# Kernel optimization log

Hardware: AMD Instinct MI355X
Metric: run time of the kernel (lower is better)

Reference implementation:

```python
import jax, jax.numpy as jnp
import numpy as np

EMBED_DIM = 1024
NUM_HEADS = 16
HEAD_DIM = EMBED_DIM // NUM_HEADS
BATCH = 2
SEQ = 2048


def setup_inputs() -> dict:
    key = jax.random.key(0)
    ks = jax.random.split(key, 9)
    s = 1.0 / np.sqrt(EMBED_DIM)
    return {
        "x": jax.random.normal(ks[0], (BATCH, SEQ, EMBED_DIM), jnp.float32),
        "mask": jnp.ones((BATCH, SEQ), jnp.int32),
        "Wq": jax.random.normal(ks[1], (EMBED_DIM, EMBED_DIM), jnp.float32) * s,
        "bq": jax.random.normal(ks[2], (EMBED_DIM,), jnp.float32) * s,
        "Wk": jax.random.normal(ks[3], (EMBED_DIM, EMBED_DIM), jnp.float32) * s,
        "bk": jax.random.normal(ks[4], (EMBED_DIM,), jnp.float32) * s,
        "Wv": jax.random.normal(ks[5], (EMBED_DIM, EMBED_DIM), jnp.float32) * s,
        "bv": jax.random.normal(ks[6], (EMBED_DIM,), jnp.float32) * s,
        "Wo": jax.random.normal(ks[7], (EMBED_DIM, EMBED_DIM), jnp.float32) * s,
        "bo": jax.random.normal(ks[8], (EMBED_DIM,), jnp.float32) * s,
    }


def reference(x, mask, Wq, bq, Wk, bk, Wv, bv, Wo, bo):
    B, S, E = x.shape
    H, D = NUM_HEADS, HEAD_DIM
    # torch Linear: y = x @ W.T + b
    q = (x @ Wq.T + bq).reshape(B, S, H, D).transpose(0, 2, 1, 3)  # [B,H,S,D]
    k = (x @ Wk.T + bk).reshape(B, S, H, D).transpose(0, 2, 1, 3)
    v = (x @ Wv.T + bv).reshape(B, S, H, D).transpose(0, 2, 1, 3)
    scores = jnp.einsum("bhqd,bhkd->bhqk", q, k) / jnp.sqrt(jnp.float32(D))
    # mask: [B,S] -> [B,1,1,S]; fill masked positions with -1e9
    scores = jnp.where(mask[:, None, None, :] == 0, jnp.float32(-1e9), scores)
    probs = jax.nn.softmax(scores, axis=-1)
    # dropout omitted: original stores a float and would crash; eval semantics = identity
    attn = jnp.einsum("bhqk,bhkd->bhqd", probs, v)  # [B,H,S,D]
    attn = attn.transpose(0, 2, 1, 3).reshape(B, S, E)
    return attn @ Wo.T + bo
```

## Files before the change

kernel.cpp:

```cpp
#include <hip/hip_runtime.h>
#include <stdint.h>

#define S_LEN 2048
#define EMB   1024
#define NH    16
#define HD    64
#define BK 64

typedef __bf16 bf16x8 __attribute__((ext_vector_type(8)));
typedef short  short4v __attribute__((ext_vector_type(4)));
typedef unsigned int uint2v __attribute__((ext_vector_type(2)));
typedef float  floatx4 __attribute__((ext_vector_type(4)));

#if defined(__has_builtin)
#if __has_builtin(__builtin_amdgcn_mfma_f32_16x16x16bf16_1k)
#define HAVE_MFMA16 1
#endif
#if __has_builtin(__builtin_amdgcn_exp2f)
#define EXP2F __builtin_amdgcn_exp2f
#endif
#endif
#ifndef EXP2F
#define EXP2F exp2f
#endif

#define QSCALE 0.1803368801111204f

__device__ __forceinline__ unsigned short f2bf(float f) {
  unsigned u = __builtin_bit_cast(unsigned, f);
  u += 0x7fffu + ((u >> 16) & 1u);
  return (unsigned short)(u >> 16);
}
__device__ __forceinline__ unsigned short f2bf_hu(float f) {
  return (unsigned short)((__builtin_bit_cast(unsigned, f) + 0x8000u) >> 16);
}
__device__ __forceinline__ unsigned packbf2(float a, float b) {
  unsigned ua = __builtin_bit_cast(unsigned, a) + 0x8000u;
  unsigned ub = __builtin_bit_cast(unsigned, b) + 0x8000u;
  return __builtin_amdgcn_perm(ub, ua, 0x07060302);
}

__global__ __launch_bounds__(256) void cvt_all(const float* __restrict__ x,
                                               const float* __restrict__ Wq,
                                               const float* __restrict__ Wk,
                                               const float* __restrict__ Wv,
                                               const float* __restrict__ Wo,
                                               unsigned short* __restrict__ xb,
                                               unsigned short* __restrict__ Wqb,
                                               unsigned short* __restrict__ Wkb,
                                               unsigned short* __restrict__ Wvb,
                                               unsigned short* __restrict__ Wob) {
  int blk = blockIdx.x;
  const float* s; unsigned short* d; int off;
  if (blk < 4096)      { s = x;  d = xb;  off = blk; }
  else if (blk < 5120) { s = Wq; d = Wqb; off = blk - 4096; }
  else if (blk < 6144) { s = Wk; d = Wkb; off = blk - 5120; }
  else if (blk < 7168) { s = Wv; d = Wvb; off = blk - 6144; }
  else                 { s = Wo; d = Wob; off = blk - 7168; }
  int i = (off * 256 + threadIdx.x) * 4;
  float4 v = *(const float4*)(s + i);
  ushort4 o;
  o.x = f2bf(v.x); o.y = f2bf(v.y); o.z = f2bf(v.z); o.w = f2bf(v.w);
  *(ushort4*)(d + i) = o;
}

__device__ __forceinline__ void stage16(const void* g, void* l) {
  __builtin_amdgcn_global_load_lds(
      (const __attribute__((address_space(1))) void*)g,
      (__attribute__((address_space(3))) void*)l, 16, 0, 0);
}

__global__ __launch_bounds__(256, 3) void qkv_gemm(const unsigned short* __restrict__ xb,
                                                   const unsigned short* __restrict__ Wqb,
                                                   const unsigned short* __restrict__ Wkb,
                                                   const unsigned short* __restrict__ Wvb,
                                                   const float* __restrict__ bq,
                                                   const float* __restrict__ bk,
                                                   const float* __restrict__ bv,
                                                   unsigned short* __restrict__ Qb,
                                                   unsigned short* __restrict__ Kb,
                                                   unsigned short* __restrict__ Vtb) {
  __shared__ unsigned short As[128 * BK];
  __shared__ unsigned short Bs[128 * BK];
  const int z = blockIdx.z;
  const unsigned short* Bm = (z == 0) ? Wqb : (z == 1) ? Wkb : Wvb;
  const float* bias        = (z == 0) ? bq  : (z == 1) ? bk  : bv;
  unsigned short* outp     = (z == 0) ? Qb  : (z == 1) ? Kb  : Vtb;
  const float scale = (z == 0) ? QSCALE : 1.0f;
  const int mode = (z == 2) ? 2 : 1;

  const int tid  = threadIdx.x;
  const int lane = tid & 63;
  const int wave = tid >> 6;
  const int m16  = lane & 15;
  const int quad = lane >> 4;
  const int m0 = blockIdx.x * 128;
  const int n0 = blockIdx.y * 128;
  const int wrow = (wave >> 1) * 64;
  const int wcol = (wave & 1) * 64;
  const int K = 1024;

  floatx4 acc[4][4];
  for (int i = 0; i < 4; ++i)
    for (int j = 0; j < 4; ++j) acc[i][j] = floatx4{0.f, 0.f, 0.f, 0.f};

  for (int k0 = 0; k0 < K; k0 += BK) {
    __syncthreads();
    for (int i = 0; i < 4; ++i) {
      int c = i * 256 + tid;
      int row = c >> 3, col = (c & 7) << 3;
      stage16(xb + (size_t)(m0 + row) * K + k0 + col,
              (char*)As + (size_t)(i * 256 + wave * 64) * 16);
      stage16(Bm + (size_t)(n0 + row) * K + k0 + col,
              (char*)Bs + (size_t)(i * 256 + wave * 64) * 16);
    }
    __syncthreads();
    for (int kk = 0; kk < 2; ++kk) {
      bf16x8 af[4], bfr[4];
      for (int ti = 0; ti < 4; ++ti)
        af[ti] = *(const bf16x8*)(As + (wrow + ti * 16 + m16) * BK + kk * 32 + quad * 8);
      for (int tj = 0; tj < 4; ++tj)
        bfr[tj] = *(const bf16x8*)(Bs + (wcol + tj * 16 + m16) * BK + kk * 32 + quad * 8);
      for (int ti = 0; ti < 4; ++ti)
        for (int tj = 0; tj < 4; ++tj)
          acc[ti][tj] = __builtin_amdgcn_mfma_f32_16x16x32_bf16(bfr[tj], af[ti], acc[ti][tj], 0, 0, 0);
    }
  }

  if (mode == 1) {
    for (int ti = 0; ti < 4; ++ti) {
      int m = m0 + wrow + ti * 16 + m16;
      int b = m >> 11, ss = m & 2047;
      for (int tj = 0; tj < 4; ++tj) {
        int n = n0 + wcol + tj * 16 + quad * 4;
        int hh = n >> 6, d = n & 63;
        float4 b4 = *(const float4*)(bias + n);
        float v0 = (acc[ti][tj][0] + b4.x) * scale;
        float v1 = (acc[ti][tj][1] + b4.y) * scale;
        float v2 = (acc[ti][tj][2] + b4.z) * scale;
        float v3 = (acc[ti][tj][3] + b4.w) * scale;
        uint2v pk{packbf2(v0, v1), packbf2(v2, v3)};
        *(uint2v*)((unsigned short*)outp +
                   ((size_t)(b * NH + hh) * S_LEN + ss) * HD + d) = pk;
      }
    }
  } else {
    for (int tj = 0; tj < 4; ++tj)
      for (int reg = 0; reg < 4; ++reg) {
        int n = n0 + wcol + tj * 16 + quad * 4 + reg;
        int hh = n >> 6, d = n & 63;
        float bv = bias[n];
        for (int ti = 0; ti < 4; ++ti) {
          int m = m0 + wrow + ti * 16 + m16;
          int b = m >> 11, ss = m & 2047;
          ((unsigned short*)outp)[((size_t)(b * NH + hh) * HD + d) * S_LEN + ss] =
              f2bf_hu(acc[ti][tj][reg] + bv);
        }
      }
  }
}

__global__ __launch_bounds__(256, 4) void out_gemm(const unsigned short* __restrict__ Ab,
                                                   const unsigned short* __restrict__ Wob,
                                                   const float* __restrict__ bo,
                                                   float* __restrict__ out) {
  __shared__ unsigned short As[128 * BK];
  __shared__ unsigned short Bs[64 * BK];
  const int tid  = threadIdx.x;
  const int lane = tid & 63;
  const int wave = tid >> 6;
  const int m16  = lane & 15;
  const int quad = lane >> 4;
  const int m0 = blockIdx.x * 128;
  const int n0 = blockIdx.y * 64;
  const int wrow = (wave >> 1) * 64;
  const int wcol = (wave & 1) * 32;
  const int K = 1024, N = 1024;

  floatx4 acc[4][2];
  for (int i = 0; i < 4; ++i)
    for (int j = 0; j < 2; ++j) acc[i][j] = floatx4{0.f, 0.f, 0.f, 0.f};

  for (int k0 = 0; k0 < K; k0 += BK) {
    __syncthreads();
    for (int i = 0; i < 4; ++i) {
      int c = i * 256 + tid;
      int row = c >> 3, col = (c & 7) << 3;
      stage16(Ab + (size_t)(m0 + row) * K + k0 + col,
              (char*)As + (size_t)(i * 256 + wave * 64) * 16);
    }
    for (int i = 0; i < 2; ++i) {
      int c = i * 256 + tid;
      int row = c >> 3, col = (c & 7) << 3;
      stage16(Wob + (size_t)(n0 + row) * K + k0 + col,
              (char*)Bs + (size_t)(i * 256 + wave * 64) * 16);
    }
    __syncthreads();
    for (int kk = 0; kk < 2; ++kk) {
      bf16x8 af[4], bfr[2];
      for (int ti = 0; ti < 4; ++ti)
        af[ti] = *(const bf16x8*)(As + (wrow + ti * 16 + m16) * BK + kk * 32 + quad * 8);
      for (int tj = 0; tj < 2; ++tj)
        bfr[tj] = *(const bf16x8*)(Bs + (wcol + tj * 16 + m16) * BK + kk * 32 + quad * 8);
      for (int ti = 0; ti < 4; ++ti)
        for (int tj = 0; tj < 2; ++tj)
          acc[ti][tj] = __builtin_amdgcn_mfma_f32_16x16x32_bf16(af[ti], bfr[tj], acc[ti][tj], 0, 0, 0);
    }
  }

  for (int tj = 0; tj < 2; ++tj) {
    int n = n0 + wcol + tj * 16 + m16;
    float bv = bo[n];
    for (int ti = 0; ti < 4; ++ti)
      for (int reg = 0; reg < 4; ++reg) {
        int m = m0 + wrow + ti * 16 + quad * 4 + reg;
        out[(size_t)m * N + n] = acc[ti][tj][reg] + bv;
      }
  }
}

__global__ __launch_bounds__(256, 2) void attn_kernel(const unsigned short* __restrict__ Qb,
                                                      const unsigned short* __restrict__ Kb,
                                                      const unsigned short* __restrict__ Vtb,
                                                      const int* __restrict__ mask,
                                                      unsigned short* __restrict__ attnb) {
  __shared__ unsigned short Ks[2 * 128 * 64];
  __shared__ unsigned short Vts[2 * 64 * 128];
  __shared__ int zw[4];
#ifndef HAVE_MFMA16
  __shared__ unsigned short Pq[4 * 16 * 72];
#endif

  const int tid  = threadIdx.x;
  const int lane = tid & 63;
  const int wave = tid >> 6;
  const int m16  = lane & 15;
  const int quad = lane >> 4;
  const int bh = blockIdx.x;
  const int qt = blockIdx.y;
  const int b  = bh >> 4;
  const int h  = bh & 15;
  const int q0 = qt * 128;
  const size_t head = (size_t)bh * S_LEN * HD;

  bf16x8 qf[2][2];
  for (int qs = 0; qs < 2; ++qs) {
    const unsigned short* qrow = Qb + head + (size_t)(q0 + wave * 32 + qs * 16 + m16) * HD;
    qf[qs][0] = *(const bf16x8*)(qrow + quad * 8);
    qf[qs][1] = *(const bf16x8*)(qrow + 32 + quad * 8);
  }

  const int kr = lane >> 3, kc = lane & 7;
  const unsigned short* kg0 = Kb + head + (size_t)(wave * 32 + kr) * HD + ((kc ^ (kr & 7)) << 3);
  const int vd = lane >> 4;
  const int vce = (lane & 8) | ((lane & 7) ^ vd);
  const unsigned short* vg0 = Vtb + head + (size_t)(wave * 16 + vd) * S_LEN + (vce << 3);
  const unsigned short* vg1 = Vtb + head + (size_t)(wave * 16 + 4 + vd) * S_LEN + ((vce ^ 4) << 3);
  const int* mrow = mask + b * S_LEN;

#define STAGE_KV(pp, kb_)                                                      \
  {                                                                            \
    const unsigned short* ksrc = kg0 + (size_t)(kb_) * 128 * HD;               \
    char* kdst = (char*)Ks + (pp) * 16384 + wave * 4096;                       \
    stage16(ksrc,        kdst);                                                \
    stage16(ksrc + 512,  kdst + 1024);                                         \
    stage16(ksrc + 1024, kdst + 2048);                                         \
    stage16(ksrc + 1536, kdst + 3072);                                         \
    const unsigned short* ve = vg0 + (kb_) * 128;                              \
    const unsigned short* vo = vg1 + (kb_) * 128;                              \
    char* vdst = (char*)Vts + (pp) * 16384 + wave * 4096;                      \
    stage16(ve,             vdst);                                             \
    stage16(vo,             vdst + 1024);                                      \
    stage16(ve + 8 * S_LEN, vdst + 2048);                                      \
    stage16(vo + 8 * S_LEN, vdst + 3072);                                      \
  }

  float l_run[2] = {0.f, 0.f};
  floatx4 acc_o[2][4];
  for (int qs = 0; qs < 2; ++qs)
    for (int ti = 0; ti < 4; ++ti) acc_o[qs][ti] = floatx4{0.f, 0.f, 0.f, 0.f};

  {
    const int4* mp = (const int4*)(mrow + tid * 8);
    int4 a = mp[0], c4 = mp[1];
    bool z = (a.x & a.y & a.z & a.w & c4.x & c4.y & c4.z & c4.w) == 0;
    unsigned long long bal = __ballot(z);
    if (lane == 0) zw[wave] = (bal != 0ull) ? 1 : 0;
  }

  STAGE_KV(0, 0);
  __syncthreads();
  const bool anymask = (zw[0] | zw[1] | zw[2] | zw[3]) != 0;

  const int xs = m16 & 7;
  const floatx4 fz = floatx4{0.f, 0.f, 0.f, 0.f};

  for (int kb = 0; kb < 16; ++kb) {
    const int p = kb & 1;
    const unsigned short* Kp = Ks + p * (128 * 64);
    const unsigned short* Vp = Vts + p * (64 * 128);
    if (kb < 15) STAGE_KV(p ^ 1, kb + 1);

    for (int hf = 0; hf < 2; ++hf) {
      floatx4 acc_s[2][4];
      {
        bf16x8 kf[4];
        for (int tj = 0; tj < 4; ++tj)
          kf[tj] = *(const bf16x8*)&Kp[(hf * 64 + tj * 16 + m16) * 64 + ((quad ^ xs) << 3)];
        for (int tj = 0; tj < 4; ++tj) {
          acc_s[0][tj] = __builtin_amdgcn_mfma_f32_16x16x32_bf16(kf[tj], qf[0][0], fz, 0, 0, 0);
          acc_s[1][tj] = __builtin_amdgcn_mfma_f32_16x16x32_bf16(kf[tj], qf[1][0], fz, 0, 0, 0);
        }
        for (int tj = 0; tj < 4; ++tj)
          kf[tj] = *(const bf16x8*)&Kp[(hf * 64 + tj * 16 + m16) * 64 + (((4 + quad) ^ xs) << 3)];
        for (int tj = 0; tj < 4; ++tj) {
          acc_s[0][tj] = __builtin_amdgcn_mfma_f32_16x16x32_bf16(kf[tj], qf[0][1], acc_s[0][tj], 0, 0, 0);
          acc_s[1][tj] = __builtin_amdgcn_mfma_f32_16x16x32_bf16(kf[tj], qf[1][1], acc_s[1][tj], 0, 0, 0);
        }
      }

      unsigned up[2][8];
      for (int qs = 0; qs < 2; ++qs) {
        float sv[16];
        for (int t = 0; t < 4; ++t)
          for (int r = 0; r < 4; ++r) sv[t * 4 + r] = acc_s[qs][t][r];
        if (anymask) {
          for (int t = 0; t < 4; ++t)
            for (int r = 0; r < 4; ++r) {
              int idx = kb * 128 + hf * 64 + t * 16 + quad * 4 + r;
              sv[t * 4 + r] += (mrow[idx] == 0) ? -1e9f : 0.f;
            }
        }
        float sl = 0.f;
        for (int i = 0; i < 8; ++i) {
          float p0 = EXP2F(sv[2 * i]);
          float p1 = EXP2F(sv[2 * i + 1]);
          sl += p0 + p1;
          up[qs][i] = packbf2(p0, p1);
        }
        sl += __shfl_xor(sl, 16);
        sl += __shfl_xor(sl, 32);
        l_run[qs] += sl;
      }

#ifdef HAVE_MFMA16
      for (int ti = 0; ti < 4; ++ti)
        for (int c = 0; c < 4; ++c) {
          short4v vf = *(const short4v*)&Vp[(ti * 16 + m16) * 128 +
                                            (((hf * 8 + 2 * c + (quad >> 1)) ^ xs) << 3) +
                                            ((quad & 1) << 2)];
          short4v Pb0 = __builtin_bit_cast(short4v, uint2v{up[0][2 * c], up[0][2 * c + 1]});
          short4v Pb1 = __builtin_bit_cast(short4v, uint2v{up[1][2 * c], up[1][2 * c + 1]});
          acc_o[0][ti] = __builtin_amdgcn_mfma_f32_16x16x16bf16_1k(vf, Pb0, acc_o[0][ti], 0, 0, 0);
          acc_o[1][ti] = __builtin_amdgcn_mfma_f32_16x16x16bf16_1k(vf, Pb1, acc_o[1][ti], 0, 0, 0);
        }
#else
      {
        unsigned short* Pw = Pq + wave * 16 * 72;
        for (int qs = 0; qs < 2; ++qs) {
          for (int t = 0; t < 4; ++t) {
            *(unsigned*)&Pw[m16 * 72 + t * 16 + quad * 4]     = up[qs][2 * t];
            *(unsigned*)&Pw[m16 * 72 + t * 16 + quad * 4 + 2] = up[qs][2 * t + 1];
          }
          for (int kk = 0; kk < 2; ++kk) {
            bf16x8 pf = *(const bf16x8*)&Pw[m16 * 72 + kk * 32 + quad * 8];
            for (int ti = 0; ti < 4; ++ti) {
              bf16x8 vfb = *(const bf16x8*)&Vp[(ti * 16 + m16) * 128 +
                                               (((hf * 8 + kk * 4 + quad) ^ xs) << 3)];
              acc_o[qs][ti] = __builtin_amdgcn_mfma_f32_16x16x32_bf16(vfb, pf, acc_o[qs][ti], 0, 0, 0);
            }
          }
        }
      }
#endif
    }

    __syncthreads();
  }

  for (int qs = 0; qs < 2; ++qs) {
    float rl = 1.f / l_run[qs];
    int orow = q0 + wave * 32 + qs * 16 + m16;
    for (int ti = 0; ti < 4; ++ti) {
      ushort4 o;
      o.x = f2bf_hu(acc_o[qs][ti][0] * rl);
      o.y = f2bf_hu(acc_o[qs][ti][1] * rl);
      o.z = f2bf_hu(acc_o[qs][ti][2] * rl);
      o.w = f2bf_hu(acc_o[qs][ti][3] * rl);
      int e = h * HD + ti * 16 + quad * 4;
      *(ushort4*)&attnb[((size_t)(b * S_LEN + orow)) * EMB + e] = o;
    }
  }
#undef STAGE_KV
}

extern "C" void kernel_launch(void* const* d_in, const int* in_sizes, int n_in,
                              void* d_out, int out_size, void* d_ws, size_t ws_size,
                              hipStream_t stream) {
  const float* x  = (const float*)d_in[0];
  const int* mask = (const int*)d_in[1];
  const float* Wq = (const float*)d_in[2];
  const float* bq = (const float*)d_in[3];
  const float* Wk = (const float*)d_in[4];
  const float* bk = (const float*)d_in[5];
  const float* Wv = (const float*)d_in[6];
  const float* bv = (const float*)d_in[7];
  const float* Wo = (const float*)d_in[8];
  const float* bo = (const float*)d_in[9];
  float* out = (float*)d_out;

  char* ws = (char*)d_ws;
  unsigned short* xb  = (unsigned short*)(ws);
  unsigned short* Wqb = (unsigned short*)(ws + 8388608);
  unsigned short* Wkb = (unsigned short*)(ws + 10485760);
  unsigned short* Wvb = (unsigned short*)(ws + 12582912);
  unsigned short* Wob = (unsigned short*)(ws + 14680064);
  unsigned short* Qb  = (unsigned short*)(ws + 16777216);
  unsigned short* Kbb = (unsigned short*)(ws + 25165824);
  unsigned short* Vtb = (unsigned short*)(ws + 33554432);
  unsigned short* Ab  = (unsigned short*)(ws + 41943040);

  cvt_all<<<dim3(8192), dim3(256), 0, stream>>>(x, Wq, Wk, Wv, Wo, xb, Wqb, Wkb, Wvb, Wob);
  qkv_gemm<<<dim3(32, 8, 3), dim3(256), 0, stream>>>(xb, Wqb, Wkb, Wvb, bq, bk, bv, Qb, Kbb, Vtb);
  attn_kernel<<<dim3(32, 16), dim3(256), 0, stream>>>(Qb, Kbb, Vtb, mask, Ab);
  out_gemm<<<dim3(32, 16), dim3(256), 0, stream>>>(Ab, Wob, bo, out);
}
```

Measured before the change: 197.2 us.

## Shrink attention KV tile to 64 keys to raise occupancy to four blocks per CU

The attention kernel now stages 64-key K/V tiles instead of 128, which halves its shared memory, and its launch bounds ask for 4 blocks per CU instead of 2. The inner half-tile loop is removed, the swizzled staging addresses are simplified, and the per-tile row-sum shuffles are moved so the row sum is reduced once at the end. The aim is more waves in flight to hide latency and fewer cross-lane reductions. In exchange there are twice as many __syncthreads barriers, and the tighter register budget may cause spills.

```diff
diff --git a/kernel.cpp b/kernel.cpp
--- a/kernel.cpp
+++ b/kernel.cpp
@@ -219,13 +219,13 @@
   }
 }
 
-__global__ __launch_bounds__(256, 2) void attn_kernel(const unsigned short* __restrict__ Qb,
+__global__ __launch_bounds__(256, 4) void attn_kernel(const unsigned short* __restrict__ Qb,
                                                       const unsigned short* __restrict__ Kb,
                                                       const unsigned short* __restrict__ Vtb,
                                                       const int* __restrict__ mask,
                                                       unsigned short* __restrict__ attnb) {
-  __shared__ unsigned short Ks[2 * 128 * 64];
-  __shared__ unsigned short Vts[2 * 64 * 128];
+  __shared__ unsigned short Ks[2 * 64 * 64];
+  __shared__ unsigned short Vts[2 * 64 * 64];
   __shared__ int zw[4];
 #ifndef HAVE_MFMA16
   __shared__ unsigned short Pq[4 * 16 * 72];
@@ -251,28 +251,20 @@
   }
 
   const int kr = lane >> 3, kc = lane & 7;
-  const unsigned short* kg0 = Kb + head + (size_t)(wave * 32 + kr) * HD + ((kc ^ (kr & 7)) << 3);
-  const int vd = lane >> 4;
-  const int vce = (lane & 8) | ((lane & 7) ^ vd);
-  const unsigned short* vg0 = Vtb + head + (size_t)(wave * 16 + vd) * S_LEN + (vce << 3);
-  const unsigned short* vg1 = Vtb + head + (size_t)(wave * 16 + 4 + vd) * S_LEN + ((vce ^ 4) << 3);
+  const unsigned short* kg0 = Kb + head + (size_t)(wave * 16 + kr) * HD + ((kc ^ kr) << 3);
+  const unsigned short* vg0 = Vtb + head + (size_t)(wave * 16 + kr) * S_LEN + ((kc ^ kr) << 3);
   const int* mrow = mask + b * S_LEN;
 
 #define STAGE_KV(pp, kb_)                                                      \
   {                                                                            \
-    const unsigned short* ksrc = kg0 + (size_t)(kb_) * 128 * HD;               \
-    char* kdst = (char*)Ks + (pp) * 16384 + wave * 4096;                       \
-    stage16(ksrc,        kdst);                                                \
-    stage16(ksrc + 512,  kdst + 1024);                                         \
-    stage16(ksrc + 1024, kdst + 2048);                                         \
-    stage16(ksrc + 1536, kdst + 3072);                                         \
-    const unsigned short* ve = vg0 + (kb_) * 128;                              \
-    const unsigned short* vo = vg1 + (kb_) * 128;                              \
-    char* vdst = (char*)Vts + (pp) * 16384 + wave * 4096;                      \
-    stage16(ve,             vdst);                                             \
-    stage16(vo,             vdst + 1024);                                      \
-    stage16(ve + 8 * S_LEN, vdst + 2048);                                      \
-    stage16(vo + 8 * S_LEN, vdst + 3072);                                      \
+    const unsigned short* ksrc = kg0 + (size_t)(kb_) * 64 * HD;                \
+    char* kdst = (char*)Ks + (pp) * 8192 + wave * 2048;                        \
+    stage16(ksrc,           kdst);                                             \
+    stage16(ksrc + 8 * HD,  kdst + 1024);                                      \
+    const unsigned short* vsrc = vg0 + (kb_) * 64;                             \
+    char* vdst = (char*)Vts + (pp) * 8192 + wave * 2048;                       \
+    stage16(vsrc,              vdst);                                          \
+    stage16(vsrc + 8 * S_LEN,  vdst + 1024);                                   \
   }
 
   float l_run[2] = {0.f, 0.f};
@@ -295,90 +287,85 @@
   const int xs = m16 & 7;
   const floatx4 fz = floatx4{0.f, 0.f, 0.f, 0.f};
 
-  for (int kb = 0; kb < 16; ++kb) {
+  for (int kb = 0; kb < 32; ++kb) {
     const int p = kb & 1;
-    const unsigned short* Kp = Ks + p * (128 * 64);
-    const unsigned short* Vp = Vts + p * (64 * 128);
-    if (kb < 15) STAGE_KV(p ^ 1, kb + 1);
-
-    for (int hf = 0; hf < 2; ++hf) {
-      floatx4 acc_s[2][4];
-      {
-        bf16x8 kf[4];
-        for (int tj = 0; tj < 4; ++tj)
-          kf[tj] = *(const bf16x8*)&Kp[(hf * 64 + tj * 16 + m16) * 64 + ((quad ^ xs) << 3)];
-        for (int tj = 0; tj < 4; ++tj) {
-          acc_s[0][tj] = __builtin_amdgcn_mfma_f32_16x16x32_bf16(kf[tj], qf[0][0], fz, 0, 0, 0);
-          acc_s[1][tj] = __builtin_amdgcn_mfma_f32_16x16x32_bf16(kf[tj], qf[1][0], fz, 0, 0, 0);
+    const unsigned short* Kp = Ks + p * 4096;
+    const unsigned short* Vp = Vts + p * 4096;
+    if (kb < 31) STAGE_KV(p ^ 1, kb + 1);
+
+    floatx4 acc_s[2][4];
+    {
+      bf16x8 kf[4];
+      for (int tj = 0; tj < 4; ++tj)
+        kf[tj] = *(const bf16x8*)&Kp[(tj * 16 + m16) * 64 + ((quad ^ xs) << 3)];
+      for (int tj = 0; tj < 4; ++tj) {
+        acc_s[0][tj] = __builtin_amdgcn_mfma_f32_16x16x32_bf16(kf[tj], qf[0][0], fz, 0, 0, 0);
+        acc_s[1][tj] = __builtin_amdgcn_mfma_f32_16x16x32_bf16(kf[tj], qf[1][0], fz, 0, 0, 0);
+      }
+      for (int tj = 0; tj < 4; ++tj)
+        kf[tj] = *(const bf16x8*)&Kp[(tj * 16 + m16) * 64 + (((4 + quad) ^ xs) << 3)];
+      for (int tj = 0; tj < 4; ++tj) {
+        acc_s[0][tj] = __builtin_amdgcn_mfma_f32_16x16x32_bf16(kf[tj], qf[0][1], acc_s[0][tj], 0, 0, 0);
+        acc_s[1][tj] = __builtin_amdgcn_mfma_f32_16x16x32_bf16(kf[tj], qf[1][1], acc_s[1][tj], 0, 0, 0);
+      }
+    }
+
+    unsigned up[2][8];
+    for (int qs = 0; qs < 2; ++qs) {
+      if (anymask) {
+        for (int t = 0; t < 4; ++t)
+          for (int r = 0; r < 4; ++r) {
+            int idx = kb * 64 + t * 16 + quad * 4 + r;
+            acc_s[qs][t][r] += (mrow[idx] == 0) ? -1e9f : 0.f;
+          }
+      }
+      float sl = 0.f;
+      for (int i = 0; i < 8; ++i) {
+        float p0 = EXP2F(acc_s[qs][i >> 1][(i & 1) * 2]);
+        float p1 = EXP2F(acc_s[qs][i >> 1][(i & 1) * 2 + 1]);
+        sl += p0 + p1;
+        up[qs][i] = packbf2(p0, p1);
+      }
+      l_run[qs] += sl;
+    }
+
+#ifdef HAVE_MFMA16
+    for (int ti = 0; ti < 4; ++ti)
+      for (int c = 0; c < 4; ++c) {
+        short4v vf = *(const short4v*)&Vp[(ti * 16 + m16) * 64 +
+                                          (((2 * c + (quad >> 1)) ^ xs) << 3) +
+                                          ((quad & 1) << 2)];
+        short4v Pb0 = __builtin_bit_cast(short4v, uint2v{up[0][2 * c], up[0][2 * c + 1]});
+        short4v Pb1 = __builtin_bit_cast(short4v, uint2v{up[1][2 * c], up[1][2 * c + 1]});
+        acc_o[0][ti] = __builtin_amdgcn_mfma_f32_16x16x16bf16_1k(vf, Pb0, acc_o[0][ti], 0, 0, 0);
+        acc_o[1][ti] = __builtin_amdgcn_mfma_f32_16x16x16bf16_1k(vf, Pb1, acc_o[1][ti], 0, 0, 0);
+      }
+#else
+    {
+      unsigned short* Pw = Pq + wave * 16 * 72;
+      for (int qs = 0; qs < 2; ++qs) {
+        for (int t = 0; t < 4; ++t) {
+          *(unsigned*)&Pw[m16 * 72 + t * 16 + quad * 4]     = up[qs][2 * t];
+          *(unsigned*)&Pw[m16 * 72 + t * 16 + quad * 4 + 2] = up[qs][2 * t + 1];
         }
-        for (int tj = 0; tj < 4; ++tj)
-          kf[tj] = *(const bf16x8*)&Kp[(hf * 64 + tj * 16 + m16) * 64 + (((4 + quad) ^ xs) << 3)];
-        for (int tj = 0; tj < 4; ++tj) {
-          acc_s[0][tj] = __builtin_amdgcn_mfma_f32_16x16x32_bf16(kf[tj], qf[0][1], acc_s[0][tj], 0, 0, 0);
-          acc_s[1][tj] = __builtin_amdgcn_mfma_f32_16x16x32_bf16(kf[tj], qf[1][1], acc_s[1][tj], 0, 0, 0);
-        }
-      }
-
-      unsigned up[2][8];
-      for (int qs = 0; qs < 2; ++qs) {
-        float sv[16];
-        for (int t = 0; t < 4; ++t)
-          for (int r = 0; r < 4; ++r) sv[t * 4 + r] = acc_s[qs][t][r];
-        if (anymask) {
-          for (int t = 0; t < 4; ++t)
-            for (int r = 0; r < 4; ++r) {
-              int idx = kb * 128 + hf * 64 + t * 16 + quad * 4 + r;
-              sv[t * 4 + r] += (mrow[idx] == 0) ? -1e9f : 0.f;
-            }
-        }
-        float sl = 0.f;
-        for (int i = 0; i < 8; ++i) {
-          float p0 = EXP2F(sv[2 * i]);
-          float p1 = EXP2F(sv[2 * i + 1]);
-          sl += p0 + p1;
-          up[qs][i] = packbf2(p0, p1);
-        }
-        sl += __shfl_xor(sl, 16);
-        sl += __shfl_xor(sl, 32);
-        l_run[qs] += sl;
-      }
-
-#ifdef HAVE_MFMA16
-      for (int ti = 0; ti < 4; ++ti)
-        for (int c = 0; c < 4; ++c) {
-          short4v vf = *(const short4v*)&Vp[(ti * 16 + m16) * 128 +
-                                            (((hf * 8 + 2 * c + (quad >> 1)) ^ xs) << 3) +
-                                            ((quad & 1) << 2)];
-          short4v Pb0 = __builtin_bit_cast(short4v, uint2v{up[0][2 * c], up[0][2 * c + 1]});
-          short4v Pb1 = __builtin_bit_cast(short4v, uint2v{up[1][2 * c], up[1][2 * c + 1]});
-          acc_o[0][ti] = __builtin_amdgcn_mfma_f32_16x16x16bf16_1k(vf, Pb0, acc_o[0][ti], 0, 0, 0);
-          acc_o[1][ti] = __builtin_amdgcn_mfma_f32_16x16x16bf16_1k(vf, Pb1, acc_o[1][ti], 0, 0, 0);
-        }
-#else
-      {
-        unsigned short* Pw = Pq + wave * 16 * 72;
-        for (int qs = 0; qs < 2; ++qs) {
-          for (int t = 0; t < 4; ++t) {
-            *(unsigned*)&Pw[m16 * 72 + t * 16 + quad * 4]     = up[qs][2 * t];
-            *(unsigned*)&Pw[m16 * 72 + t * 16 + quad * 4 + 2] = up[qs][2 * t + 1];
-          }
-          for (int kk = 0; kk < 2; ++kk) {
-            bf16x8 pf = *(const bf16x8*)&Pw[m16 * 72 + kk * 32 + quad * 8];
-            for (int ti = 0; ti < 4; ++ti) {
-              bf16x8 vfb = *(const bf16x8*)&Vp[(ti * 16 + m16) * 128 +
-                                               (((hf * 8 + kk * 4 + quad) ^ xs) << 3)];
-              acc_o[qs][ti] = __builtin_amdgcn_mfma_f32_16x16x32_bf16(vfb, pf, acc_o[qs][ti], 0, 0, 0);
-            }
+        for (int kk = 0; kk < 2; ++kk) {
+          bf16x8 pf = *(const bf16x8*)&Pw[m16 * 72 + kk * 32 + quad * 8];
+          for (int ti = 0; ti < 4; ++ti) {
+            bf16x8 vfb = *(const bf16x8*)&Vp[(ti * 16 + m16) * 64 +
+                                             (((kk * 4 + quad) ^ xs) << 3)];
+            acc_o[qs][ti] = __builtin_amdgcn_mfma_f32_16x16x32_bf16(vfb, pf, acc_o[qs][ti], 0, 0, 0);
           }
         }
       }
-#endif
-    }
+    }
+#endif
 
     __syncthreads();
   }
 
   for (int qs = 0; qs < 2; ++qs) {
+    l_run[qs] += __shfl_xor(l_run[qs], 16);
+    l_run[qs] += __shfl_xor(l_run[qs], 32);
     float rl = 1.f / l_run[qs];
     int orow = q0 + wave * 32 + qs * 16 + m16;
     for (int ti = 0; ti < 4; ++ti) {
```

Measured after the change: 199.0 us. Within noise of the previous version (+0.9%).
